# Optimization experiments

Measured on AMD Instinct MI355X. Metric: run time of the kernel, lower is better.

## Reference

```python
import jax, jax.numpy as jnp
import numpy as np
from jax.scipy.special import logsumexp


def setup_inputs() -> dict:
    key = jax.random.key(0)
    k = jax.random.split(key, 8)
    B, T, K, L = 32, 128, 16, 16
    s = 0.05
    y_batch = jax.random.uniform(k[0], (B, T, 1, 28, 28), dtype=jnp.float32)
    enc_w1 = jax.random.normal(k[1], (400, 784), dtype=jnp.float32) * s
    enc_b1 = jnp.zeros((400,), jnp.float32)
    enc_w2 = jax.random.normal(k[2], (2 * L, 400), dtype=jnp.float32) * s
    enc_b2 = jnp.zeros((2 * L,), jnp.float32)
    dec_fc_w = jax.random.normal(k[3], (400, L + K), dtype=jnp.float32) * s
    dec_fc_b = jnp.zeros((400,), jnp.float32)
    dec_w = jax.random.normal(k[4], (784, 400), dtype=jnp.float32) * s
    dec_b = jnp.zeros((784,), jnp.float32)
    log_pi = jnp.zeros((K,), jnp.float32)
    log_A = jax.random.normal(k[5], (K, K), dtype=jnp.float32)
    log_A = log_A.at[jnp.arange(K), jnp.arange(K)].set(-1e9)  # fill_diagonal_(-1e9)
    eps = jax.random.normal(k[6], (B * T, L), dtype=jnp.float32)
    return dict(y_batch=y_batch, enc_w1=enc_w1, enc_b1=enc_b1, enc_w2=enc_w2,
                enc_b2=enc_b2, dec_fc_w=dec_fc_w, dec_fc_b=dec_fc_b, dec_w=dec_w,
                dec_b=dec_b, log_pi=log_pi, log_A=log_A, eps=eps)


def reference(y_batch, enc_w1, enc_b1, enc_w2, enc_b2, dec_fc_w, dec_fc_b,
              dec_w, dec_b, log_pi, log_A, eps):
    B, T = y_batch.shape[0], y_batch.shape[1]
    K = log_pi.shape[0]
    L = eps.shape[1]
    N = B * T
    # ---- VAE emission log-likelihoods (compute_log_bk); dropout in eval mode ----
    y_flat = y_batch.reshape(N, 784)
    h = jax.nn.relu(y_flat @ enc_w1.T + enc_b1)                 # [N,400]
    ml = h @ enc_w2.T + enc_b2                                   # [N,2L]
    mu, logvar = ml[:, :L], ml[:, L:]
    z = mu + eps * jnp.exp(0.5 * logvar)                         # reparameterize
    # decode(z, one_hot(k)) for all k at once: split cat-linear into z part + k column
    Wz, Wx = dec_fc_w[:, :L], dec_fc_w[:, L:]                    # [400,L],[400,K]
    base = z @ Wz.T + dec_fc_b                                   # [N,400]
    hk = jax.nn.relu(base[None, :, :] + Wx.T[:, None, :])        # [K,N,400]
    y_rec = jax.nn.sigmoid(jnp.einsum('knh,oh->kno', hk, dec_w) + dec_b)  # [K,N,784]
    # binary_cross_entropy with torch's log clamp at -100
    logp = jnp.clip(jnp.log(y_rec), -100.0, None)
    log1mp = jnp.clip(jnp.log(1.0 - y_rec), -100.0, None)
    bce = -(y_flat[None] * logp + (1.0 - y_flat[None]) * log1mp)  # [K,N,784]
    recon = bce.sum(-1) / 100.0                                   # [K,N]
    log_bk = (-recon).reshape(K, B, T).transpose(1, 2, 0)         # [B,T,K]
    # ---- forward-backward in log domain ----
    lp = jnp.log(jax.nn.softmax(log_pi) + 1e-9)
    lA = jnp.log(jax.nn.softmax(log_A, axis=1) + 1e-9)
    lb_rest = jnp.moveaxis(log_bk[:, 1:], 1, 0)                   # [T-1,B,K]
    a0 = lp + log_bk[:, 0]                                        # [B,K]

    def fstep(prev, lb_t):
        cur = logsumexp(prev[:, :, None] + lA[None], axis=1) + lb_t
        return cur, cur

    _, alphas = jax.lax.scan(fstep, a0, lb_rest)
    log_alpha = jnp.concatenate([a0[:, None], jnp.moveaxis(alphas, 0, 1)], axis=1)  # [B,T,K]

    bT = jnp.zeros((B, K), log_bk.dtype)

    def bstep(nxt, lb_t1):
        cur = logsumexp(lA[None] + (lb_t1 + nxt)[:, None, :], axis=2)
        return cur, cur

    _, betas = jax.lax.scan(bstep, bT, lb_rest, reverse=True)     # betas[t] = beta_t, t=0..T-2
    log_beta = jnp.concatenate([jnp.moveaxis(betas, 0, 1), bT[:, None]], axis=1)  # [B,T,K]

    lg = log_alpha + log_beta
    log_gamma = lg - logsumexp(lg, axis=2, keepdims=True)

    lxi = (log_alpha[:, :-1, :, None] + lA[None, None]
           + (log_bk[:, 1:] + log_beta[:, 1:])[:, :, None, :])    # [B,T-1,K,K]
    lxi = lxi - logsumexp(lxi, axis=(2, 3), keepdims=True)
    return jnp.exp(log_gamma), jnp.exp(lxi)
```

## Files before the change

### kernel.cpp

```cpp
#include <hip/hip_runtime.h>
#include <math.h>


typedef _Float16 h8v __attribute__((ext_vector_type(8)));
typedef _Float16 h4v __attribute__((ext_vector_type(4)));
typedef float f16v __attribute__((ext_vector_type(16)));

__device__ __forceinline__ void gll16(const void* g, void* l) {
  __builtin_amdgcn_global_load_lds(
      (const __attribute__((address_space(1))) void*)g,
      (__attribute__((address_space(3))) void*)l, 16, 0, 0);
}

__global__ __launch_bounds__(256)
void k_prep(const float* __restrict__ dw, const float* __restrict__ ew1,
            _Float16* __restrict__ dwh, _Float16* __restrict__ w1h,
            float* __restrict__ lb) {
  int idx = blockIdx.x * 256 + threadIdx.x;
  if (idx < 65536) lb[idx] = 0.f;
  if (idx < 896 * 448) {
    int o = idx / 448, h2 = idx - o * 448;
    float v = (o < 784 && h2 < 400) ? dw[o * 400 + h2] : 0.f;
    dwh[idx] = (_Float16)v;
  } else if (idx < 896 * 448 + 512 * 800) {
    int j = idx - 896 * 448;
    int i = j / 800, kc = j - i * 800;
    float v = (i < 400 && kc < 784) ? ew1[i * 784 + kc] : 0.f;
    w1h[j] = (_Float16)v;
  }
}

#define E1ST 40
__global__ __launch_bounds__(256, 2)
void k_enc1(const float* __restrict__ y, const _Float16* __restrict__ w1h,
            const float* __restrict__ b1, float* __restrict__ hout) {
  __shared__ __align__(16) _Float16 Ah[64 * E1ST];
  __shared__ __align__(16) _Float16 Bh[128 * E1ST];
  const int tid = threadIdx.x;
  const int i0 = blockIdx.x * 128;
  const int n0 = blockIdx.y * 64;
  const int wav = tid >> 6, lane = tid & 63;
  const int wn = wav >> 1, wi = wav & 1;
  const int ln = lane & 31, kg = lane >> 5;

  f16v acc[2];
#pragma unroll
  for (int j = 0; j < 2; ++j)
#pragma unroll
    for (int r = 0; r < 16; ++r) acc[j][r] = 0.f;

  const int ar = tid >> 3, ac4 = (tid & 7) * 4;
  const int br = tid >> 2, bg = (tid & 3) * 8;

#pragma unroll 1
  for (int hc = 0; hc < 25; ++hc) {
    const int h0 = hc * 32;
    __syncthreads();
#pragma unroll
    for (int it = 0; it < 2; ++it) {
      int r = ar + 32 * it;
      float4 a = make_float4(0.f, 0.f, 0.f, 0.f);
      if (h0 + ac4 < 784) a = *(const float4*)&y[(n0 + r) * 784 + h0 + ac4];
      h4v hv;
      hv[0] = (_Float16)a.x; hv[1] = (_Float16)a.y;
      hv[2] = (_Float16)a.z; hv[3] = (_Float16)a.w;
      *(h4v*)&Ah[r * E1ST + ac4] = hv;
    }
#pragma unroll
    for (int it = 0; it < 2; ++it) {
      int r = br + 64 * it;
      *(h8v*)&Bh[r * E1ST + bg] = *(const h8v*)&w1h[(i0 + r) * 800 + h0 + bg];
    }
    __syncthreads();
#pragma unroll
    for (int kk = 0; kk < 2; ++kk) {
      const int ko = kk * 16 + kg * 8;
      h8v a  = *(const h8v*)&Ah[(wn * 32 + ln) * E1ST + ko];
      h8v b0 = *(const h8v*)&Bh[(wi * 64 + ln) * E1ST + ko];
      h8v b1 = *(const h8v*)&Bh[(wi * 64 + 32 + ln) * E1ST + ko];
      acc[0] = __builtin_amdgcn_mfma_f32_32x32x16_f16(a, b0, acc[0], 0, 0, 0);
      acc[1] = __builtin_amdgcn_mfma_f32_32x32x16_f16(a, b1, acc[1], 0, 0, 0);
    }
  }
#pragma unroll
  for (int j = 0; j < 2; ++j) {
    const int i = i0 + wi * 64 + j * 32 + ln;
    if (i < 400) {
      const float bias = b1[i];
#pragma unroll
      for (int reg = 0; reg < 16; ++reg) {
        const int row = n0 + wn * 32 + (reg & 3) + 8 * (reg >> 2) + 4 * kg;
        hout[row * 400 + i] = fmaxf(acc[j][reg] + bias, 0.f);
      }
    }
  }
}

__global__ __launch_bounds__(128, 2)
void k_enc2z(const float* __restrict__ h, const float* __restrict__ w2,
             const float* __restrict__ b2, const float* __restrict__ eps,
             float* __restrict__ z) {
  __shared__ __align__(16) float h_lds[16 * 400];
  __shared__ __align__(16) float w2_lds[32 * 404];
  __shared__ float ml_lds[16 * 32];
  const int tid = threadIdx.x;
  const int n0 = blockIdx.x * 16;
  for (int idx = tid; idx < 1600; idx += 128) {
    int r = idx / 100, c = idx - r * 100;
    *(float4*)&h_lds[r * 400 + c * 4] = *(const float4*)&h[(n0 + r) * 400 + c * 4];
  }
  for (int idx = tid; idx < 3200; idx += 128) {
    int r = idx / 100, c = idx - r * 100;
    *(float4*)&w2_lds[r * 404 + c * 4] = *(const float4*)&w2[r * 400 + c * 4];
  }
  __syncthreads();
  const int c_ = tid & 31, n4 = tid >> 5;
  float a0 = 0.f, a1 = 0.f, a2 = 0.f, a3 = 0.f;
  for (int q = 0; q < 100; ++q) {
    float4 wv = *(const float4*)&w2_lds[c_ * 404 + q * 4];
    float4 h0 = *(const float4*)&h_lds[(n4 * 4 + 0) * 400 + q * 4];
    float4 h1 = *(const float4*)&h_lds[(n4 * 4 + 1) * 400 + q * 4];
    float4 h2 = *(const float4*)&h_lds[(n4 * 4 + 2) * 400 + q * 4];
    float4 h3 = *(const float4*)&h_lds[(n4 * 4 + 3) * 400 + q * 4];
    a0 += h0.x * wv.x + h0.y * wv.y + h0.z * wv.z + h0.w * wv.w;
    a1 += h1.x * wv.x + h1.y * wv.y + h1.z * wv.z + h1.w * wv.w;
    a2 += h2.x * wv.x + h2.y * wv.y + h2.z * wv.z + h2.w * wv.w;
    a3 += h3.x * wv.x + h3.y * wv.y + h3.z * wv.z + h3.w * wv.w;
  }
  const float bb = b2[c_];
  ml_lds[(n4 * 4 + 0) * 32 + c_] = a0 + bb;
  ml_lds[(n4 * 4 + 1) * 32 + c_] = a1 + bb;
  ml_lds[(n4 * 4 + 2) * 32 + c_] = a2 + bb;
  ml_lds[(n4 * 4 + 3) * 32 + c_] = a3 + bb;
  __syncthreads();
  for (int t = tid; t < 256; t += 128) {
    int n2 = t >> 4, l = t & 15;
    float mu = ml_lds[n2 * 32 + l];
    float lv = ml_lds[n2 * 32 + 16 + l];
    z[(n0 + n2) * 16 + l] = mu + eps[(n0 + n2) * 16 + l] * expf(0.5f * lv);
  }
}

__global__ __launch_bounds__(256, 4)
void k_base(const float* __restrict__ z, const float* __restrict__ dfw,
            const float* __restrict__ dfb, float* __restrict__ basep) {
  __shared__ float z_lds[16 * 16];
  __shared__ __align__(16) float wz_lds[400 * 20];
  const int tid = threadIdx.x;
  const int n0 = blockIdx.x * 16;
  if (tid < 64) {
    int n = tid >> 2, c = (tid & 3) * 4;
    *(float4*)&z_lds[n * 16 + c] = *(const float4*)&z[(n0 + n) * 16 + c];
  }
  for (int idx = tid; idx < 1600; idx += 256) {
    int i = idx >> 2, c = (idx & 3) * 4;
    *(float4*)&wz_lds[i * 20 + c] = *(const float4*)&dfw[i * 32 + c];
  }
  __syncthreads();
  for (int idx = tid; idx < 7168; idx += 256) {
    int n = idx / 448, i = idx - n * 448;
    float acc = 0.f;
    if (i < 400) {
      acc = dfb[i];
#pragma unroll
      for (int q = 0; q < 4; ++q) {
        float4 zv = *(const float4*)&z_lds[n * 16 + q * 4];
        float4 wv = *(const float4*)&wz_lds[i * 20 + q * 4];
        acc += zv.x * wv.x + zv.y * wv.y + zv.z * wv.z + zv.w * wv.w;
      }
    }
    basep[(n0 + n) * 448 + i] = acc;
  }
}

__global__ __launch_bounds__(256, 4)
void k_hk(const float* __restrict__ basep, const float* __restrict__ dfw,
          _Float16* __restrict__ hkh) {
  __shared__ float wxT[16 * 448];
  const int tid = threadIdx.x;
  const int n0 = blockIdx.x * 8;
  for (int idx = tid; idx < 7168; idx += 256) {
    int k = idx / 448, hh = idx - k * 448;
    wxT[idx] = (hh < 400) ? dfw[hh * 32 + 16 + k] : 0.f;
  }
  __syncthreads();
  for (int s = tid; s < 448; s += 256) {
    int r = s / 56, c8 = s - r * 56;
    const float* bp = &basep[(size_t)(n0 + r) * 448 + c8 * 8];
    float4 b0 = *(const float4*)bp;
    float4 b1 = *(const float4*)(bp + 4);
#pragma unroll
    for (int k = 0; k < 16; ++k) {
      const float* wp = &wxT[k * 448 + c8 * 8];
      float4 w0 = *(const float4*)wp;
      float4 w1 = *(const float4*)(wp + 4);
      h8v o;
      o[0] = (_Float16)fmaxf(b0.x + w0.x, 0.f);
      o[1] = (_Float16)fmaxf(b0.y + w0.y, 0.f);
      o[2] = (_Float16)fmaxf(b0.z + w0.z, 0.f);
      o[3] = (_Float16)fmaxf(b0.w + w0.w, 0.f);
      o[4] = (_Float16)fmaxf(b1.x + w1.x, 0.f);
      o[5] = (_Float16)fmaxf(b1.y + w1.y, 0.f);
      o[6] = (_Float16)fmaxf(b1.z + w1.z, 0.f);
      o[7] = (_Float16)fmaxf(b1.w + w1.w, 0.f);
      *(h8v*)&hkh[((size_t)k * 4096 + n0 + r) * 448 + c8 * 8] = o;
    }
  }
}

__global__ __launch_bounds__(256, 2)
void k_dec3(const _Float16* __restrict__ hkh, const _Float16* __restrict__ dwh,
            const float* __restrict__ decb, const float* __restrict__ y,
            float* __restrict__ lb) {
  __shared__ __align__(16) _Float16 AhB[2][128 * 64];
  __shared__ __align__(16) _Float16 Bh[128 * 64];
  __shared__ float red[256];

  const int tid = threadIdx.x;
  const int id  = blockIdx.x;
  const int lin = (id & 7) * 448 + (id >> 3);
  const int n_i = lin / 112;
  const int rem = lin - n_i * 112;
  const int k   = rem / 7;
  const int ot  = rem - k * 7;
  const int n0  = n_i * 128;
  const int o0  = ot * 128;

  const int wav = tid >> 6, lane = tid & 63;
  const int wn = wav >> 1, wo = wav & 1;
  const int ln = lane & 31, kg = lane >> 5;

  const int l8 = lane >> 3, l7 = lane & 7;
  const int swh = (l7 * 8) ^ (l8 * 8);
  const _Float16* hkk = hkh + (size_t)k * (4096 * 448);
  const _Float16* pA[4];
  const _Float16* pB[4];
#pragma unroll
  for (int i = 0; i < 4; ++i) {
    const int row = wav * 32 + i * 8 + l8;
    pA[i] = hkk + (size_t)(n0 + row) * 448 + swh;
    pB[i] = dwh + (size_t)(o0 + row) * 448 + swh;
  }

  f16v acc[2][2];
#pragma unroll
  for (int i = 0; i < 2; ++i)
#pragma unroll
    for (int j = 0; j < 2; ++j)
#pragma unroll
      for (int r = 0; r < 16; ++r) acc[i][j][r] = 0.f;

#pragma unroll
  for (int i = 0; i < 4; ++i) { gll16(pA[i], &AhB[0][(wav * 4 + i) * 512]); pA[i] += 64; }
#pragma unroll
  for (int i = 0; i < 4; ++i) { gll16(pB[i], &Bh[(wav * 4 + i) * 512]);     pB[i] += 64; }
#pragma unroll
  for (int i = 0; i < 4; ++i) { gll16(pA[i], &AhB[1][(wav * 4 + i) * 512]); pA[i] += 64; }
  asm volatile("s_waitcnt vmcnt(4)" ::: "memory");
  __builtin_amdgcn_sched_barrier(0);
  __builtin_amdgcn_s_barrier();

  const int sx = (ln & 7) * 8;
  const int e0 = (kg * 8) ^ sx;
  const int arow = (wn * 64 + ln) * 64;
  const int brow = (wo * 64 + ln) * 64;

  int cur = 0;
#pragma unroll 1
  for (int hc = 0; hc < 7; ++hc) {
    const _Float16* Ac = AhB[cur];
#pragma unroll
    for (int kk = 0; kk < 4; ++kk) {
      const int cx = (kk * 16) ^ e0;
      h8v a0 = *(const h8v*)&Ac[arow + cx];
      h8v a1 = *(const h8v*)&Ac[arow + 2048 + cx];
      h8v b0 = *(const h8v*)&Bh[brow + cx];
      h8v b1 = *(const h8v*)&Bh[brow + 2048 + cx];
      acc[0][0] = __builtin_amdgcn_mfma_f32_32x32x16_f16(a0, b0, acc[0][0], 0, 0, 0);
      acc[1][0] = __builtin_amdgcn_mfma_f32_32x32x16_f16(a1, b0, acc[1][0], 0, 0, 0);
      acc[0][1] = __builtin_amdgcn_mfma_f32_32x32x16_f16(a0, b1, acc[0][1], 0, 0, 0);
      acc[1][1] = __builtin_amdgcn_mfma_f32_32x32x16_f16(a1, b1, acc[1][1], 0, 0, 0);
    }
    if (hc == 6) break;
    __builtin_amdgcn_s_barrier();
#pragma unroll
    for (int i = 0; i < 4; ++i) { gll16(pB[i], &Bh[(wav * 4 + i) * 512]); pB[i] += 64; }
    if (hc < 5) {
#pragma unroll
      for (int i = 0; i < 4; ++i) { gll16(pA[i], &AhB[cur][(wav * 4 + i) * 512]); pA[i] += 64; }
      asm volatile("s_waitcnt vmcnt(4)" ::: "memory");
    } else {
      asm volatile("s_waitcnt vmcnt(0)" ::: "memory");
    }
    __builtin_amdgcn_sched_barrier(0);
    __builtin_amdgcn_s_barrier();
    cur ^= 1;
  }

  const int obase = o0 + wo * 64;
  const float bj0 = (obase + ln < 784) ? decb[obase + ln] : 0.f;
  const float bj1 = (obase + 32 + ln < 784) ? decb[obase + 32 + ln] : 0.f;
#pragma unroll
  for (int i = 0; i < 2; ++i) {
#pragma unroll
    for (int reg = 0; reg < 16; ++reg) {
      const int row = wn * 64 + i * 32 + (reg & 3) + 8 * (reg >> 2) + 4 * kg;
      float v = 0.f;
#pragma unroll
      for (int j = 0; j < 2; ++j) {
        const int o = obase + j * 32 + ln;
        if (o < 784) {
          float x = acc[i][j][reg] + (j ? bj1 : bj0);
          float yv = y[(n0 + row) * 784 + o];
          float spx = fmaxf(x, 0.f) + __logf(1.f + __expf(-fabsf(x)));
          v += spx - yv * x;
        }
      }
      v += __shfl_xor(v, 1, 64);
      v += __shfl_xor(v, 2, 64);
      v += __shfl_xor(v, 4, 64);
      v += __shfl_xor(v, 8, 64);
      v += __shfl_xor(v, 16, 64);
      if (ln == 0) red[wo * 128 + row] = v;
    }
  }
  __syncthreads();
  if (tid < 128) {
    float s = red[tid] + red[128 + tid];
    atomicAdd(&lb[(n0 + tid) * 16 + k], s);
  }
}

#define DST 72
__global__ __launch_bounds__(256, 2)
void k_dec1(const float* __restrict__ basep, const float* __restrict__ dfw,
            const _Float16* __restrict__ dwh, const float* __restrict__ decb,
            const float* __restrict__ y, float* __restrict__ lb) {
  __shared__ __align__(16) _Float16 Ah[128 * DST];
  __shared__ __align__(16) _Float16 Bh[128 * DST];
  __shared__ float wx[448];
  __shared__ float red[256];

  const int tid = threadIdx.x;
  const int id  = blockIdx.x;
  const int lin = (id & 7) * 448 + (id >> 3);
  const int n_i = lin / 112;
  const int rem = lin - n_i * 112;
  const int k   = rem / 7;
  const int ot  = rem - k * 7;
  const int n0  = n_i * 128;
  const int o0  = ot * 128;
  const bool full = (ot < 6);

  const int wav = tid >> 6, lane = tid & 63;
  const int wn = wav >> 1, wo = wav & 1;
  const int ln = lane & 31, kg = lane >> 5;

  for (int i = tid; i < 448; i += 256) wx[i] = (i < 400) ? dfw[i * 32 + 16 + k] : 0.f;

  const int ar = tid >> 4, ac4 = (tid & 15) * 4;
  const int br = tid >> 3, bg = (tid & 7) * 8;
  const float* aptr = basep + (long)(n0 + ar) * 448 + ac4;

  float4 apf[8];
#pragma unroll
  for (int it = 0; it < 8; ++it) apf[it] = *(const float4*)&aptr[(16 * it) * 448];

  f16v acc[2][2];
#pragma unroll
  for (int i = 0; i < 2; ++i)
#pragma unroll
    for (int j = 0; j < 2; ++j)
#pragma unroll
      for (int r = 0; r < 16; ++r) acc[i][j][r] = 0.f;

#pragma unroll 1
  for (int hc = 0; hc < 7; ++hc) {
    const int h0 = hc * 64;
    h8v bpf[4];
#pragma unroll
    for (int it = 0; it < 4; ++it)
      bpf[it] = *(const h8v*)&dwh[(o0 + br + 32 * it) * 448 + h0 + bg];
    __syncthreads();
    {
      float4 w = *(const float4*)&wx[h0 + ac4];
#pragma unroll
      for (int it = 0; it < 8; ++it) {
        int r = ar + 16 * it;
        h4v hv;
        hv[0] = (_Float16)fmaxf(apf[it].x + w.x, 0.f);
        hv[1] = (_Float16)fmaxf(apf[it].y + w.y, 0.f);
        hv[2] = (_Float16)fmaxf(apf[it].z + w.z, 0.f);
        hv[3] = (_Float16)fmaxf(apf[it].w + w.w, 0.f);
        *(h4v*)&Ah[r * DST + ac4] = hv;
      }
    }
#pragma unroll
    for (int it = 0; it < 4; ++it)
      *(h8v*)&Bh[(br + 32 * it) * DST + bg] = bpf[it];
    __syncthreads();
    if (hc < 6) {
      const int hn = (hc + 1) * 64;
#pragma unroll
      for (int it = 0; it < 8; ++it)
        apf[it] = *(const float4*)&aptr[(16 * it) * 448 + hn];
    }
#pragma unroll
    for (int kk = 0; kk < 4; ++kk) {
      const int ko = kk * 16 + kg * 8;
      h8v a0 = *(const h8v*)&Ah[(wn * 64 + ln) * DST + ko];
      h8v a1 = *(const h8v*)&Ah[(wn * 64 + 32 + ln) * DST + ko];
      h8v b0 = *(const h8v*)&Bh[(wo * 64 + ln) * DST + ko];
      h8v b1 = *(const h8v*)&Bh[(wo * 64 + 32 + ln) * DST + ko];
      if (full) {
        acc[0][0] = __builtin_amdgcn_mfma_f32_32x32x16_f16(a0, b0, acc[0][0], 0, 0, 0);
        acc[1][0] = __builtin_amdgcn_mfma_f32_32x32x16_f16(a1, b0, acc[1][0], 0, 0, 0);
        acc[0][1] = __builtin_amdgcn_mfma_f32_32x32x16_f16(a0, b1, acc[0][1], 0, 0, 0);
        acc[1][1] = __builtin_amdgcn_mfma_f32_32x32x16_f16(a1, b1, acc[1][1], 0, 0, 0);
      } else if (wo == 0) {
        acc[0][0] = __builtin_amdgcn_mfma_f32_32x32x16_f16(a0, b0, acc[0][0], 0, 0, 0);
        acc[1][0] = __builtin_amdgcn_mfma_f32_32x32x16_f16(a1, b0, acc[1][0], 0, 0, 0);
      }
    }
  }
  const int obase = o0 + wo * 64;
  const float bj0 = (obase + ln < 784) ? decb[obase + ln] : 0.f;
  const float bj1 = (obase + 32 + ln < 784) ? decb[obase + 32 + ln] : 0.f;
#pragma unroll
  for (int i = 0; i < 2; ++i) {
#pragma unroll
    for (int reg = 0; reg < 16; ++reg) {
      const int row = wn * 64 + i * 32 + (reg & 3) + 8 * (reg >> 2) + 4 * kg;
      float v = 0.f;
#pragma unroll
      for (int j = 0; j < 2; ++j) {
        const int o = obase + j * 32 + ln;
        if (o < 784) {
          float x = acc[i][j][reg] + (j ? bj1 : bj0);
          float yv = y[(n0 + row) * 784 + o];
          float spx = fmaxf(x, 0.f) + __logf(1.f + __expf(-fabsf(x)));
          float t2 = fminf(spx, 100.f);
          float t1 = fminf(spx - x, 100.f);
          v += t2 + yv * (t1 - t2);
        }
      }
      v += __shfl_xor(v, 1, 64);
      v += __shfl_xor(v, 2, 64);
      v += __shfl_xor(v, 4, 64);
      v += __shfl_xor(v, 8, 64);
      v += __shfl_xor(v, 16, 64);
      if (ln == 0) red[wo * 128 + row] = v;
    }
  }
  __syncthreads();
  if (tid < 128) {
    float s = red[tid] + red[128 + tid];
    atomicAdd(&lb[(n0 + tid) * 16 + k], s);
  }
}

__global__ __launch_bounds__(256, 2)
void k_hmm(const float* __restrict__ lb, const float* __restrict__ lpi,
           const float* __restrict__ lA, float* __restrict__ out,
           float* __restrict__ g_ah, float* __restrict__ g_pb,
           float* __restrict__ g_sinv, float* __restrict__ g_Al) {
  __shared__ float btl[128 * 16];
  __shared__ float ah[128 * 16];
  __shared__ float bh[128 * 16];
  __shared__ float braw[128 * 16];
  __shared__ float A_l[16 * 17];
  __shared__ float pi_l[16];
  const int tid = threadIdx.x;
  const int b = blockIdx.x;

  for (int idx = tid; idx < 512; idx += 256) {
    float4 v = *(const float4*)&lb[b * 2048 + idx * 4];
    v.x *= -0.01f; v.y *= -0.01f; v.z *= -0.01f; v.w *= -0.01f;
    *(float4*)&btl[idx * 4] = v;
  }
  if (tid < 16) {
    const int j = tid;
    float m = -1e30f;
#pragma unroll
    for (int q = 0; q < 16; ++q) m = fmaxf(m, lA[j * 16 + q]);
    float e[16]; float s = 0.f;
#pragma unroll
    for (int q = 0; q < 16; ++q) { e[q] = expf(lA[j * 16 + q] - m); s += e[q]; }
    float inv = 1.f / s;
#pragma unroll
    for (int q = 0; q < 16; ++q) {
      float v = e[q] * inv + 1e-9f;
      A_l[j * 17 + q] = v;
      g_Al[j * 16 + q] = v;
    }
  } else if (tid == 16) {
    float m = -1e30f;
#pragma unroll
    for (int q = 0; q < 16; ++q) m = fmaxf(m, lpi[q]);
    float e[16]; float s = 0.f;
#pragma unroll
    for (int q = 0; q < 16; ++q) { e[q] = expf(lpi[q] - m); s += e[q]; }
    float inv = 1.f / s;
#pragma unroll
    for (int q = 0; q < 16; ++q) pi_l[q] = e[q] * inv + 1e-9f;
  }
  __syncthreads();
  if (tid < 128) {
    const int t = tid;
    float v[16]; float m = -1e30f;
#pragma unroll
    for (int q = 0; q < 16; ++q) { v[q] = btl[t * 16 + q]; m = fmaxf(m, v[q]); }
#pragma unroll
    for (int q = 0; q < 16; ++q) btl[t * 16 + q] = expf(v[q] - m);
  }
  __syncthreads();
  const int lane = tid & 63;
  const int kk = lane & 15, grp = lane >> 4;
  if (tid < 64) {
    float v0 = pi_l[kk] * btl[kk];
    float ss0 = v0;
    ss0 += __shfl_xor(ss0, 1, 64); ss0 += __shfl_xor(ss0, 2, 64);
    ss0 += __shfl_xor(ss0, 4, 64); ss0 += __shfl_xor(ss0, 8, 64);
    if (grp == 0) ah[kk] = v0 / ss0;
    for (int t = 1; t < 128; ++t) {
      float acc = 0.f;
#pragma unroll
      for (int jj = 0; jj < 4; ++jj) {
        int j = grp * 4 + jj;
        acc = fmaf(ah[(t - 1) * 16 + j], A_l[j * 17 + kk], acc);
      }
      acc += __shfl_xor(acc, 16, 64);
      acc += __shfl_xor(acc, 32, 64);
      float v = acc * btl[t * 16 + kk];
      float ss = v;
      ss += __shfl_xor(ss, 1, 64); ss += __shfl_xor(ss, 2, 64);
      ss += __shfl_xor(ss, 4, 64); ss += __shfl_xor(ss, 8, 64);
      if (grp == 0) ah[t * 16 + kk] = v / ss;
    }
  } else if (tid < 128) {
    if (grp == 0) bh[127 * 16 + kk] = 1.f;
    for (int t = 126; t >= 0; --t) {
      float acc = 0.f;
#pragma unroll
      for (int q = 0; q < 4; ++q) {
        int k2 = grp * 4 + q;
        acc = fmaf(A_l[kk * 17 + k2], btl[(t + 1) * 16 + k2] * bh[(t + 1) * 16 + k2], acc);
      }
      acc += __shfl_xor(acc, 16, 64);
      acc += __shfl_xor(acc, 32, 64);
      float ss = acc;
      ss += __shfl_xor(ss, 1, 64); ss += __shfl_xor(ss, 2, 64);
      ss += __shfl_xor(ss, 4, 64); ss += __shfl_xor(ss, 8, 64);
      if (grp == 0) { braw[t * 16 + kk] = acc; bh[t * 16 + kk] = acc / ss; }
    }
  }
  __syncthreads();
  if (tid < 128) {
    const int t = tid;
    float g[16]; float s2 = 0.f;
#pragma unroll
    for (int q = 0; q < 16; ++q) { g[q] = ah[t * 16 + q] * bh[t * 16 + q]; s2 += g[q]; }
    float inv = 1.f / s2;
#pragma unroll
    for (int c = 0; c < 4; ++c) {
      float4 o;
      o.x = g[c * 4 + 0] * inv; o.y = g[c * 4 + 1] * inv;
      o.z = g[c * 4 + 2] * inv; o.w = g[c * 4 + 3] * inv;
      *(float4*)&out[(b * 128 + t) * 16 + c * 4] = o;
      float4 av = *(float4*)&ah[t * 16 + c * 4];
      *(float4*)&g_ah[(b * 128 + t) * 16 + c * 4] = av;
      float4 p;
      p.x = btl[t * 16 + c * 4 + 0] * bh[t * 16 + c * 4 + 0];
      p.y = btl[t * 16 + c * 4 + 1] * bh[t * 16 + c * 4 + 1];
      p.z = btl[t * 16 + c * 4 + 2] * bh[t * 16 + c * 4 + 2];
      p.w = btl[t * 16 + c * 4 + 3] * bh[t * 16 + c * 4 + 3];
      *(float4*)&g_pb[(b * 128 + t) * 16 + c * 4] = p;
    }
  } else {
    const int t = tid - 128;
    if (t < 127) {
      float s2 = 0.f;
#pragma unroll
      for (int q = 0; q < 16; ++q) s2 += ah[t * 16 + q] * braw[t * 16 + q];
      g_sinv[b * 128 + t] = 1.f / s2;
    }
  }
}

__global__ __launch_bounds__(256)
void k_xi(const float* __restrict__ g_ah, const float* __restrict__ g_pb,
          const float* __restrict__ g_sinv, const float* __restrict__ g_Al,
          float* __restrict__ out) {
  const int b = blockIdx.x, t = blockIdx.y;
  const int tid = threadIdx.x;
  const int j = tid >> 4, k2 = tid & 15;
  float val = g_ah[(b * 128 + t) * 16 + j] * g_Al[j * 16 + k2] *
              g_pb[(b * 128 + t + 1) * 16 + k2] * g_sinv[b * 128 + t];
  out[65536 + (b * 127 + t) * 256 + tid] = val;
}

extern "C" void kernel_launch(void* const* d_in, const int* in_sizes, int n_in,
                              void* d_out, int out_size, void* d_ws, size_t ws_size,
                              hipStream_t stream) {
  (void)in_sizes; (void)n_in; (void)out_size;
  const float* y   = (const float*)d_in[0];
  const float* ew1 = (const float*)d_in[1];
  const float* eb1 = (const float*)d_in[2];
  const float* ew2 = (const float*)d_in[3];
  const float* eb2 = (const float*)d_in[4];
  const float* dfw = (const float*)d_in[5];
  const float* dfb = (const float*)d_in[6];
  const float* dw  = (const float*)d_in[7];
  const float* db  = (const float*)d_in[8];
  const float* lpi = (const float*)d_in[9];
  const float* lA  = (const float*)d_in[10];
  const float* eps = (const float*)d_in[11];
  float* out = (float*)d_out;

  float* ws = (float*)d_ws;
  float* h      = ws;
  float* basep  = ws;
  float* z      = ws + 1835008;
  float* lb     = z + 65536;
  _Float16* dwh = (_Float16*)(lb + 65536);
  _Float16* w1h = dwh + 896 * 448;
  float* g_ah   = (float*)(w1h + 512 * 800);
  float* g_pb   = g_ah + 65536;
  float* g_sinv = g_pb + 65536;
  float* g_Al   = g_sinv + 4096;
  _Float16* hkh = (_Float16*)(g_Al + 256);

  const bool big_ws = (ws_size >= 68748288ull);

  k_prep<<<3168, 256, 0, stream>>>(dw, ew1, dwh, w1h, lb);
  k_enc1<<<dim3(4, 64), 256, 0, stream>>>(y, w1h, eb1, h);
  k_enc2z<<<256, 128, 0, stream>>>(h, ew2, eb2, eps, z);
  k_base<<<256, 256, 0, stream>>>(z, dfw, dfb, basep);
  if (big_ws) {
    k_hk<<<512, 256, 0, stream>>>(basep, dfw, hkh);
    k_dec3<<<3584, 256, 0, stream>>>(hkh, dwh, db, y, lb);
  } else {
    k_dec1<<<3584, 256, 0, stream>>>(basep, dfw, dwh, db, y, lb);
  }
  k_hmm<<<32, 256, 0, stream>>>(lb, lpi, lA, out, g_ah, g_pb, g_sinv, g_Al);
  k_xi<<<dim3(32, 127), 256, 0, stream>>>(g_ah, g_pb, g_sinv, g_Al, out);
}
```

Baseline: 364.0 us.

## Fuse base+hk kernels, double-buffer decoder B tile, fold xi into HMM kernel

Merges the decoder base projection and per-state hidden expansion into one kernel that keeps the base activations in LDS, so the fp32 base buffer no longer round-trips through global memory and one launch disappears. The decoder GEMM now double-buffers both A and B tiles and issues the next chunk's loads before computing the current one, replacing the older scheme where only A was double-buffered. The xi output is computed inside the HMM kernel straight from LDS, removing the separate xi launch and its intermediate global buffers. The cost is that only 32 blocks now write the large xi tensor serially over time steps, and the GEMM uses more LDS.

```diff
diff --git a/kernel.cpp b/kernel.cpp
--- a/kernel.cpp
+++ b/kernel.cpp
@@ -141,6 +141,63 @@
   }
 }
 
+__global__ __launch_bounds__(256, 2)
+void k_basehk(const float* __restrict__ z, const float* __restrict__ dfw,
+              const float* __restrict__ dfb, _Float16* __restrict__ hkh) {
+  __shared__ float z_lds[16 * 16];
+  __shared__ __align__(16) float wz[400 * 20];
+  __shared__ __align__(16) float base[16 * 448];
+  const int tid = threadIdx.x;
+  const int n0 = blockIdx.x * 16;
+  if (tid < 64) {
+    int n = tid >> 2, c = (tid & 3) * 4;
+    *(float4*)&z_lds[n * 16 + c] = *(const float4*)&z[(n0 + n) * 16 + c];
+  }
+  for (int idx = tid; idx < 1600; idx += 256) {
+    int i = idx >> 2, c = (idx & 3) * 4;
+    *(float4*)&wz[i * 20 + c] = *(const float4*)&dfw[i * 32 + c];
+  }
+  __syncthreads();
+  for (int idx = tid; idx < 7168; idx += 256) {
+    int n = idx / 448, i = idx - n * 448;
+    float acc = 0.f;
+    if (i < 400) {
+      acc = dfb[i];
+#pragma unroll
+      for (int q = 0; q < 4; ++q) {
+        float4 zv = *(const float4*)&z_lds[n * 16 + q * 4];
+        float4 wv = *(const float4*)&wz[i * 20 + q * 4];
+        acc += zv.x * wv.x + zv.y * wv.y + zv.z * wv.z + zv.w * wv.w;
+      }
+    }
+    base[n * 448 + i] = acc;
+  }
+  __syncthreads();
+  for (int idx = tid; idx < 7168; idx += 256) {
+    int k = idx / 448, hh = idx - k * 448;
+    wz[idx] = (hh < 400) ? dfw[hh * 32 + 16 + k] : 0.f;
+  }
+  __syncthreads();
+  for (int s = tid; s < 14336; s += 256) {
+    int k = s / 896, r2 = s - k * 896;
+    int r = r2 / 56, c8 = r2 - r * 56;
+    const float* bp = &base[r * 448 + c8 * 8];
+    const float* wp = &wz[k * 448 + c8 * 8];
+    float4 b0 = *(const float4*)bp, b1 = *(const float4*)(bp + 4);
+    float4 w0 = *(const float4*)wp, w1 = *(const float4*)(wp + 4);
+    h8v o;
+    o[0] = (_Float16)fmaxf(b0.x + w0.x, 0.f);
+    o[1] = (_Float16)fmaxf(b0.y + w0.y, 0.f);
+    o[2] = (_Float16)fmaxf(b0.z + w0.z, 0.f);
+    o[3] = (_Float16)fmaxf(b0.w + w0.w, 0.f);
+    o[4] = (_Float16)fmaxf(b1.x + w1.x, 0.f);
+    o[5] = (_Float16)fmaxf(b1.y + w1.y, 0.f);
+    o[6] = (_Float16)fmaxf(b1.z + w1.z, 0.f);
+    o[7] = (_Float16)fmaxf(b1.w + w1.w, 0.f);
+    *(h8v*)&hkh[((size_t)k * 4096 + n0 + r) * 448 + c8 * 8] = o;
+  }
+}
+
 __global__ __launch_bounds__(256, 4)
 void k_base(const float* __restrict__ z, const float* __restrict__ dfw,
             const float* __restrict__ dfb, float* __restrict__ basep) {
@@ -173,47 +230,12 @@
   }
 }
 
-__global__ __launch_bounds__(256, 4)
-void k_hk(const float* __restrict__ basep, const float* __restrict__ dfw,
-          _Float16* __restrict__ hkh) {
-  __shared__ float wxT[16 * 448];
-  const int tid = threadIdx.x;
-  const int n0 = blockIdx.x * 8;
-  for (int idx = tid; idx < 7168; idx += 256) {
-    int k = idx / 448, hh = idx - k * 448;
-    wxT[idx] = (hh < 400) ? dfw[hh * 32 + 16 + k] : 0.f;
-  }
-  __syncthreads();
-  for (int s = tid; s < 448; s += 256) {
-    int r = s / 56, c8 = s - r * 56;
-    const float* bp = &basep[(size_t)(n0 + r) * 448 + c8 * 8];
-    float4 b0 = *(const float4*)bp;
-    float4 b1 = *(const float4*)(bp + 4);
-#pragma unroll
-    for (int k = 0; k < 16; ++k) {
-      const float* wp = &wxT[k * 448 + c8 * 8];
-      float4 w0 = *(const float4*)wp;
-      float4 w1 = *(const float4*)(wp + 4);
-      h8v o;
-      o[0] = (_Float16)fmaxf(b0.x + w0.x, 0.f);
-      o[1] = (_Float16)fmaxf(b0.y + w0.y, 0.f);
-      o[2] = (_Float16)fmaxf(b0.z + w0.z, 0.f);
-      o[3] = (_Float16)fmaxf(b0.w + w0.w, 0.f);
-      o[4] = (_Float16)fmaxf(b1.x + w1.x, 0.f);
-      o[5] = (_Float16)fmaxf(b1.y + w1.y, 0.f);
-      o[6] = (_Float16)fmaxf(b1.z + w1.z, 0.f);
-      o[7] = (_Float16)fmaxf(b1.w + w1.w, 0.f);
-      *(h8v*)&hkh[((size_t)k * 4096 + n0 + r) * 448 + c8 * 8] = o;
-    }
-  }
-}
-
 __global__ __launch_bounds__(256, 2)
-void k_dec3(const _Float16* __restrict__ hkh, const _Float16* __restrict__ dwh,
+void k_dec5(const _Float16* __restrict__ hkh, const _Float16* __restrict__ dwh,
             const float* __restrict__ decb, const float* __restrict__ y,
             float* __restrict__ lb) {
-  __shared__ __align__(16) _Float16 AhB[2][128 * 64];
-  __shared__ __align__(16) _Float16 Bh[128 * 64];
+  __shared__ __align__(16) _Float16 Ah[2][128 * 64];
+  __shared__ __align__(16) _Float16 Bh[2][128 * 64];
   __shared__ float red[256];
 
   const int tid = threadIdx.x;
@@ -251,50 +273,47 @@
       for (int r = 0; r < 16; ++r) acc[i][j][r] = 0.f;
 
 #pragma unroll
-  for (int i = 0; i < 4; ++i) { gll16(pA[i], &AhB[0][(wav * 4 + i) * 512]); pA[i] += 64; }
-#pragma unroll
-  for (int i = 0; i < 4; ++i) { gll16(pB[i], &Bh[(wav * 4 + i) * 512]);     pB[i] += 64; }
-#pragma unroll
-  for (int i = 0; i < 4; ++i) { gll16(pA[i], &AhB[1][(wav * 4 + i) * 512]); pA[i] += 64; }
-  asm volatile("s_waitcnt vmcnt(4)" ::: "memory");
+  for (int i = 0; i < 4; ++i) { gll16(pA[i], &Ah[0][(wav * 4 + i) * 512]); pA[i] += 64; }
+#pragma unroll
+  for (int i = 0; i < 4; ++i) { gll16(pB[i], &Bh[0][(wav * 4 + i) * 512]); pB[i] += 64; }
+  asm volatile("s_waitcnt vmcnt(0)" ::: "memory");
   __builtin_amdgcn_sched_barrier(0);
   __builtin_amdgcn_s_barrier();
 
-  const int sx = (ln & 7) * 8;
-  const int e0 = (kg * 8) ^ sx;
+  const int e0 = (kg * 8) ^ ((ln & 7) * 8);
   const int arow = (wn * 64 + ln) * 64;
   const int brow = (wo * 64 + ln) * 64;
 
   int cur = 0;
 #pragma unroll 1
   for (int hc = 0; hc < 7; ++hc) {
-    const _Float16* Ac = AhB[cur];
+    if (hc < 6) {
+#pragma unroll
+      for (int i = 0; i < 4; ++i) { gll16(pA[i], &Ah[cur ^ 1][(wav * 4 + i) * 512]); pA[i] += 64; }
+#pragma unroll
+      for (int i = 0; i < 4; ++i) { gll16(pB[i], &Bh[cur ^ 1][(wav * 4 + i) * 512]); pB[i] += 64; }
+      __builtin_amdgcn_sched_barrier(0);
+    }
+    const _Float16* Ac = Ah[cur];
+    const _Float16* Bc = Bh[cur];
 #pragma unroll
     for (int kk = 0; kk < 4; ++kk) {
       const int cx = (kk * 16) ^ e0;
       h8v a0 = *(const h8v*)&Ac[arow + cx];
       h8v a1 = *(const h8v*)&Ac[arow + 2048 + cx];
-      h8v b0 = *(const h8v*)&Bh[brow + cx];
-      h8v b1 = *(const h8v*)&Bh[brow + 2048 + cx];
+      h8v b0 = *(const h8v*)&Bc[brow + cx];
+      h8v b1 = *(const h8v*)&Bc[brow + 2048 + cx];
       acc[0][0] = __builtin_amdgcn_mfma_f32_32x32x16_f16(a0, b0, acc[0][0], 0, 0, 0);
       acc[1][0] = __builtin_amdgcn_mfma_f32_32x32x16_f16(a1, b0, acc[1][0], 0, 0, 0);
       acc[0][1] = __builtin_amdgcn_mfma_f32_32x32x16_f16(a0, b1, acc[0][1], 0, 0, 0);
       acc[1][1] = __builtin_amdgcn_mfma_f32_32x32x16_f16(a1, b1, acc[1][1], 0, 0, 0);
     }
-    if (hc == 6) break;
-    __builtin_amdgcn_s_barrier();
-#pragma unroll
-    for (int i = 0; i < 4; ++i) { gll16(pB[i], &Bh[(wav * 4 + i) * 512]); pB[i] += 64; }
-    if (hc < 5) {
-#pragma unroll
-      for (int i = 0; i < 4; ++i) { gll16(pA[i], &AhB[cur][(wav * 4 + i) * 512]); pA[i] += 64; }
-      asm volatile("s_waitcnt vmcnt(4)" ::: "memory");
-    } else {
+    if (hc < 6) {
       asm volatile("s_waitcnt vmcnt(0)" ::: "memory");
-    }
-    __builtin_amdgcn_sched_barrier(0);
-    __builtin_amdgcn_s_barrier();
-    cur ^= 1;
+      __builtin_amdgcn_sched_barrier(0);
+      __builtin_amdgcn_s_barrier();
+      cur ^= 1;
+    }
   }
 
   const int obase = o0 + wo * 64;
@@ -461,15 +480,14 @@
 
 __global__ __launch_bounds__(256, 2)
 void k_hmm(const float* __restrict__ lb, const float* __restrict__ lpi,
-           const float* __restrict__ lA, float* __restrict__ out,
-           float* __restrict__ g_ah, float* __restrict__ g_pb,
-           float* __restrict__ g_sinv, float* __restrict__ g_Al) {
+           const float* __restrict__ lA, float* __restrict__ out) {
   __shared__ float btl[128 * 16];
   __shared__ float ah[128 * 16];
   __shared__ float bh[128 * 16];
   __shared__ float braw[128 * 16];
   __shared__ float A_l[16 * 17];
   __shared__ float pi_l[16];
+  __shared__ float sinv_l[128];
   const int tid = threadIdx.x;
   const int b = blockIdx.x;
 
@@ -488,11 +506,7 @@
     for (int q = 0; q < 16; ++q) { e[q] = expf(lA[j * 16 + q] - m); s += e[q]; }
     float inv = 1.f / s;
 #pragma unroll
-    for (int q = 0; q < 16; ++q) {
-      float v = e[q] * inv + 1e-9f;
-      A_l[j * 17 + q] = v;
-      g_Al[j * 16 + q] = v;
-    }
+    for (int q = 0; q < 16; ++q) A_l[j * 17 + q] = e[q] * inv + 1e-9f;
   } else if (tid == 16) {
     float m = -1e30f;
 #pragma unroll
@@ -567,14 +581,6 @@
       o.x = g[c * 4 + 0] * inv; o.y = g[c * 4 + 1] * inv;
       o.z = g[c * 4 + 2] * inv; o.w = g[c * 4 + 3] * inv;
       *(float4*)&out[(b * 128 + t) * 16 + c * 4] = o;
-      float4 av = *(float4*)&ah[t * 16 + c * 4];
-      *(float4*)&g_ah[(b * 128 + t) * 16 + c * 4] = av;
-      float4 p;
-      p.x = btl[t * 16 + c * 4 + 0] * bh[t * 16 + c * 4 + 0];
-      p.y = btl[t * 16 + c * 4 + 1] * bh[t * 16 + c * 4 + 1];
-      p.z = btl[t * 16 + c * 4 + 2] * bh[t * 16 + c * 4 + 2];
-      p.w = btl[t * 16 + c * 4 + 3] * bh[t * 16 + c * 4 + 3];
-      *(float4*)&g_pb[(b * 128 + t) * 16 + c * 4] = p;
     }
   } else {
     const int t = tid - 128;
@@ -582,21 +588,18 @@
       float s2 = 0.f;
 #pragma unroll
       for (int q = 0; q < 16; ++q) s2 += ah[t * 16 + q] * braw[t * 16 + q];
-      g_sinv[b * 128 + t] = 1.f / s2;
-    }
-  }
-}
-
-__global__ __launch_bounds__(256)
-void k_xi(const float* __restrict__ g_ah, const float* __restrict__ g_pb,
-          const float* __restrict__ g_sinv, const float* __restrict__ g_Al,
-          float* __restrict__ out) {
-  const int b = blockIdx.x, t = blockIdx.y;
-  const int tid = threadIdx.x;
+      sinv_l[t] = 1.f / s2;
+    }
+  }
+  __syncthreads();
   const int j = tid >> 4, k2 = tid & 15;
-  float val = g_ah[(b * 128 + t) * 16 + j] * g_Al[j * 16 + k2] *
-              g_pb[(b * 128 + t + 1) * 16 + k2] * g_sinv[b * 128 + t];
-  out[65536 + (b * 127 + t) * 256 + tid] = val;
+  const float aj = A_l[j * 17 + k2];
+  float* xo = out + 65536 + (size_t)b * 127 * 256 + tid;
+  for (int t = 0; t < 127; ++t) {
+    float val = ah[t * 16 + j] * aj * btl[(t + 1) * 16 + k2] *
+                bh[(t + 1) * 16 + k2] * sinv_l[t];
+    xo[t * 256] = val;
+  }
 }
 
 extern "C" void kernel_launch(void* const* d_in, const int* in_sizes, int n_in,
@@ -624,24 +627,20 @@
   float* lb     = z + 65536;
   _Float16* dwh = (_Float16*)(lb + 65536);
   _Float16* w1h = dwh + 896 * 448;
-  float* g_ah   = (float*)(w1h + 512 * 800);
-  float* g_pb   = g_ah + 65536;
-  float* g_sinv = g_pb + 65536;
-  float* g_Al   = g_sinv + 4096;
-  _Float16* hkh = (_Float16*)(g_Al + 256);
+  float* gpad   = (float*)(w1h + 512 * 800);
+  _Float16* hkh = (_Float16*)(gpad + 65536 * 2 + 4096 + 256);
 
   const bool big_ws = (ws_size >= 68748288ull);
 
   k_prep<<<3168, 256, 0, stream>>>(dw, ew1, dwh, w1h, lb);
   k_enc1<<<dim3(4, 64), 256, 0, stream>>>(y, w1h, eb1, h);
   k_enc2z<<<256, 128, 0, stream>>>(h, ew2, eb2, eps, z);
-  k_base<<<256, 256, 0, stream>>>(z, dfw, dfb, basep);
   if (big_ws) {
-    k_hk<<<512, 256, 0, stream>>>(basep, dfw, hkh);
-    k_dec3<<<3584, 256, 0, stream>>>(hkh, dwh, db, y, lb);
+    k_basehk<<<256, 256, 0, stream>>>(z, dfw, dfb, hkh);
+    k_dec5<<<3584, 256, 0, stream>>>(hkh, dwh, db, y, lb);
   } else {
+    k_base<<<256, 256, 0, stream>>>(z, dfw, dfb, basep);
     k_dec1<<<3584, 256, 0, stream>>>(basep, dfw, dwh, db, y, lb);
   }
-  k_hmm<<<32, 256, 0, stream>>>(lb, lpi, lA, out, g_ah, g_pb, g_sinv, g_Al);
-  k_xi<<<dim3(32, 127), 256, 0, stream>>>(g_ah, g_pb, g_sinv, g_Al, out);
-}
+  k_hmm<<<32, 256, 0, stream>>>(lb, lpi, lA, out);
+}
```

Result: slower. 375.2 us (+3.1%).
